# Performance work log

Measured on AMD Instinct MI355X. Metric: run time of the kernel, lower is better.

## Reference

```python
import jax, jax.numpy as jnp
import numpy as np

B, S, D, N, H = 4, 1024, 768, 12, 64
IGNORE = -100000.0


def setup_inputs() -> dict:
    key = jax.random.key(0)
    ks = jax.random.split(key, 9)
    std = 0.02
    return {
        "normalized_resid_pre": jax.random.normal(ks[0], (B, S, D), dtype=jnp.float32),
        "W_Q": jax.random.normal(ks[1], (N, D, H), dtype=jnp.float32) * std,
        "W_K": jax.random.normal(ks[2], (N, D, H), dtype=jnp.float32) * std,
        "W_V": jax.random.normal(ks[3], (N, D, H), dtype=jnp.float32) * std,
        "W_O": jax.random.normal(ks[4], (N, H, D), dtype=jnp.float32) * std,
        "b_Q": jnp.zeros((N, H), dtype=jnp.float32),
        "b_K": jnp.zeros((N, H), dtype=jnp.float32),
        "b_V": jnp.zeros((N, H), dtype=jnp.float32),
        "b_O": jnp.zeros((D,), dtype=jnp.float32),
    }


def reference(normalized_resid_pre, W_Q, W_K, W_V, W_O, b_Q, b_K, b_V, b_O):
    x = normalized_resid_pre  # [b, s, d]
    d_head = W_Q.shape[-1]
    # per-head projections: [b, n, s, h]
    Q = jnp.einsum("bsd,ndh->bnsh", x, W_Q) + b_Q[None, :, None, :]
    K = jnp.einsum("bsd,ndh->bnsh", x, W_K) + b_K[None, :, None, :]
    V = jnp.einsum("bsd,ndh->bnsh", x, W_V) + b_V[None, :, None, :]
    # scores [b, n, s_q, s_k]
    scores = jnp.einsum("bnqh,bnkh->bnqk", Q, K) / jnp.sqrt(jnp.float32(d_head))
    s = scores.shape[-1]
    # original: tril(scores) + triu(IGNORE, k=1) == where(causal, scores, IGNORE)
    causal = jnp.tril(jnp.ones((s, s), dtype=bool))
    masked = jnp.where(causal[None, None], scores, jnp.float32(IGNORE))
    probs = jax.nn.softmax(masked, axis=-1)
    # z [b, s_q, n, h]
    z = jnp.einsum("bnqk,bnkh->bqnh", probs, V)
    out = jnp.einsum("bqnh,nhd->bqd", z, W_O) + b_O
    return out
```

## Files before the change

kernel.cpp:

```cpp
#include <hip/hip_runtime.h>

typedef __bf16 bf16x8 __attribute__((ext_vector_type(8)));
typedef __bf16 bf16x4 __attribute__((ext_vector_type(4)));
typedef float  f32x4  __attribute__((ext_vector_type(4)));

constexpr int B_ = 4, S_ = 1024, D_ = 768, N_ = 12, H_ = 64;
constexpr int BNSH = B_ * N_ * S_ * H_;
constexpr float SCALE2 = 0.18033688011f;

__device__ __forceinline__ f32x4 mfma16(bf16x8 a, bf16x8 b, f32x4 c) {
    return __builtin_amdgcn_mfma_f32_16x16x32_bf16(a, b, c, 0, 0, 0);
}

__device__ __forceinline__ void gload16(const __bf16* g, __bf16* l) {
    __builtin_amdgcn_global_load_lds(
        (const __attribute__((address_space(1))) unsigned int*)g,
        (__attribute__((address_space(3))) unsigned int*)l, 16, 0, 0);
}

__device__ __forceinline__ void stage128x64(const __bf16* g, int ld, __bf16* lds,
                                            int wid, int lane) {
    #pragma unroll
    for (int i = 0; i < 4; ++i) {
        int cb = (wid * 4 + i) * 64;
        int chunk = cb + lane;
        int r = chunk >> 3, p = chunk & 7;
        int q = p ^ (r & 7);
        gload16(g + (size_t)r * ld + q * 8, lds + cb * 8);
    }
}
__device__ __forceinline__ void stage64x64(const __bf16* g, int ld, __bf16* lds,
                                           int wid, int lane) {
    #pragma unroll
    for (int i = 0; i < 2; ++i) {
        int cb = (wid * 2 + i) * 64;
        int chunk = cb + lane;
        int r = chunk >> 3, p = chunk & 7;
        int q = p ^ (r & 7);
        gload16(g + (size_t)r * ld + q * 8, lds + cb * 8);
    }
}

__global__ __launch_bounds__(256) void prep_kernel(
    const float* __restrict__ x,
    const float* __restrict__ wq, const float* __restrict__ wk,
    const float* __restrict__ wv, const float* __restrict__ wo,
    __bf16* __restrict__ xb, __bf16* __restrict__ wt, __bf16* __restrict__ wot) {
    __shared__ __bf16 T[64][65];
    const int blk = blockIdx.x;
    const int tid = threadIdx.x;
    if (blk < 768) {
        int base = blk * 1024 + tid;
        #pragma unroll
        for (int i = 0; i < 4; ++i) {
            int idx = base + i * 256;
            float4 v = ((const float4*)x)[idx];
            bf16x4 o;
            o[0] = (__bf16)v.x; o[1] = (__bf16)v.y;
            o[2] = (__bf16)v.z; o[3] = (__bf16)v.w;
            ((bf16x4*)xb)[idx] = o;
        }
        return;
    }
    int rr = tid >> 4, c4 = (tid & 15) * 4;
    if (blk < 1200) {
        int t = blk - 768;
        int dt = t % 12, mh = t / 12;
        int mat = mh / 12, n = mh % 12;
        const float* in = (mat == 0 ? wq : mat == 1 ? wk : wv) + (size_t)n * 768 * 64;
        __bf16* outp = wt + (size_t)(mat * 768 + n * 64) * 768;
        int d0 = dt * 64;
        #pragma unroll
        for (int i = 0; i < 4; ++i) {
            int row = rr + 16 * i;
            float4 v = *(const float4*)&in[(size_t)(d0 + row) * 64 + c4];
            T[c4 + 0][row] = (__bf16)v.x;
            T[c4 + 1][row] = (__bf16)v.y;
            T[c4 + 2][row] = (__bf16)v.z;
            T[c4 + 3][row] = (__bf16)v.w;
        }
        __syncthreads();
        #pragma unroll
        for (int i = 0; i < 4; ++i) {
            int hrow = rr + 16 * i;
            bf16x4 o;
            o[0] = T[hrow][c4 + 0]; o[1] = T[hrow][c4 + 1];
            o[2] = T[hrow][c4 + 2]; o[3] = T[hrow][c4 + 3];
            *(bf16x4*)&outp[(size_t)hrow * 768 + d0 + c4] = o;
        }
    } else {
        int t = blk - 1200;
        int r0 = (t % 12) * 64, c0 = (t / 12) * 64;
        #pragma unroll
        for (int i = 0; i < 4; ++i) {
            int row = rr + 16 * i;
            float4 v = *(const float4*)&wo[(size_t)(r0 + row) * 768 + c0 + c4];
            T[c4 + 0][row] = (__bf16)v.x;
            T[c4 + 1][row] = (__bf16)v.y;
            T[c4 + 2][row] = (__bf16)v.z;
            T[c4 + 3][row] = (__bf16)v.w;
        }
        __syncthreads();
        #pragma unroll
        for (int i = 0; i < 4; ++i) {
            int crow = rr + 16 * i;
            bf16x4 o;
            o[0] = T[crow][c4 + 0]; o[1] = T[crow][c4 + 1];
            o[2] = T[crow][c4 + 2]; o[3] = T[crow][c4 + 3];
            *(bf16x4*)&wot[(size_t)(c0 + crow) * 768 + r0 + c4] = o;
        }
    }
}

__global__ __launch_bounds__(256) void qkv_gemm(
    const __bf16* __restrict__ xb, const __bf16* __restrict__ wtg,
    const float* __restrict__ bq, const float* __restrict__ bk,
    const float* __restrict__ bv,
    __bf16* __restrict__ Qb, __bf16* __restrict__ Kb, __bf16* __restrict__ Vtb) {
    __shared__ __bf16 As[2][128 * 64];
    __shared__ __bf16 Bs[2][64 * 64];
    const int m0 = blockIdx.x * 128;
    const int j0 = blockIdx.y * 64;
    const int tid = threadIdx.x, wid = tid >> 6, lane = tid & 63;
    const int quad = lane >> 4, lrow = lane & 15;
    const int l3 = lrow & 7;
    int koff[2];
    #pragma unroll
    for (int ks = 0; ks < 2; ++ks)
        koff[ks] = lrow * 64 + ((ks * 4 + quad) ^ l3) * 8;

    f32x4 zf = {0.f, 0.f, 0.f, 0.f};
    f32x4 acc[2][4];
    #pragma unroll
    for (int i = 0; i < 2; ++i)
        #pragma unroll
        for (int j = 0; j < 4; ++j) acc[i][j] = zf;

    stage128x64(xb + (size_t)m0 * 768, 768, As[0], wid, lane);
    stage64x64(wtg + (size_t)j0 * 768, 768, Bs[0], wid, lane);

    for (int kt = 0; kt < 12; ++kt) {
        const int buf = kt & 1;
        __syncthreads();
        if (kt < 11) {
            stage128x64(xb + (size_t)m0 * 768 + (kt + 1) * 64, 768, As[buf ^ 1], wid, lane);
            stage64x64(wtg + (size_t)j0 * 768 + (kt + 1) * 64, 768, Bs[buf ^ 1], wid, lane);
        }
        #pragma unroll
        for (int ks = 0; ks < 2; ++ks) {
            bf16x8 af[2], bfr[4];
            #pragma unroll
            for (int mi = 0; mi < 2; ++mi)
                af[mi] = *(const bf16x8*)(As[buf] + (wid * 32 + mi * 16) * 64 + koff[ks]);
            #pragma unroll
            for (int ni = 0; ni < 4; ++ni)
                bfr[ni] = *(const bf16x8*)(Bs[buf] + ni * 1024 + koff[ks]);
            #pragma unroll
            for (int mi = 0; mi < 2; ++mi)
                #pragma unroll
                for (int ni = 0; ni < 4; ++ni)
                    acc[mi][ni] = mfma16(af[mi], bfr[ni], acc[mi][ni]);
        }
    }

    const int mat = j0 / 768;
    const int n = (j0 % 768) >> 6;
    const int b = m0 >> 10;
    const int s_base = (m0 & 1023) + wid * 32;
    const float* bias = (mat == 0 ? bq : mat == 1 ? bk : bv) + n * 64;
    const float osc = (mat == 0) ? SCALE2 : 1.0f;
    float bias_v[4];
    #pragma unroll
    for (int ni = 0; ni < 4; ++ni) bias_v[ni] = bias[ni * 16 + lrow];

    if (mat == 2) {
        __bf16* vout = Vtb + (size_t)(b * N_ + n) * 64 * 1024;
        #pragma unroll
        for (int mi = 0; mi < 2; ++mi)
            #pragma unroll
            for (int ni = 0; ni < 4; ++ni) {
                int h = ni * 16 + lrow;
                int s0 = s_base + mi * 16 + quad * 4;
                bf16x4 pv;
                #pragma unroll
                for (int r = 0; r < 4; ++r)
                    pv[r] = (__bf16)(acc[mi][ni][r] + bias_v[ni]);
                *(bf16x4*)(vout + (size_t)h * 1024 + s0) = pv;
            }
    } else {
        __bf16* qk = (mat == 0 ? Qb : Kb) + (size_t)(b * N_ + n) * 1024 * 64;
        #pragma unroll
        for (int mi = 0; mi < 2; ++mi)
            #pragma unroll
            for (int r = 0; r < 4; ++r) {
                int s = s_base + mi * 16 + quad * 4 + r;
                #pragma unroll
                for (int ni = 0; ni < 4; ++ni)
                    qk[(size_t)s * 64 + ni * 16 + lrow] =
                        (__bf16)((acc[mi][ni][r] + bias_v[ni]) * osc);
            }
    }
}

__global__ __launch_bounds__(256) void attn_mfma(
    const __bf16* __restrict__ Qb, const __bf16* __restrict__ Kb,
    const __bf16* __restrict__ Vtb, __bf16* __restrict__ zb) {
    __shared__ __bf16 Ks[2][64 * 64], Vs[2][64 * 64];
    __shared__ __bf16 Pt[4][16 * 64];
    const int bid = blockIdx.x;
    const int qt = 15 - bid / 48;
    const int bn = bid % 48;
    const int b = bn / N_, n = bn % N_;
    const int tid = threadIdx.x, wid = tid >> 6, lane = tid & 63;
    const int quad = lane >> 4, lrow = lane & 15;
    const int l3 = lrow & 7;
    const __bf16* Qg = Qb + (size_t)(b * N_ + n) * S_ * H_;
    const __bf16* Kg = Kb + (size_t)(b * N_ + n) * S_ * H_;
    const __bf16* Vg = Vtb + (size_t)(b * N_ + n) * H_ * S_;
    const int q0 = qt * 64;

    int koff[2];
    #pragma unroll
    for (int ks = 0; ks < 2; ++ks)
        koff[ks] = lrow * 64 + ((ks * 4 + quad) ^ l3) * 8;
    int ptw[4], ptr_[2];
    #pragma unroll
    for (int nt = 0; nt < 4; ++nt) {
        int c16 = nt * 2 + (quad >> 1);
        ptw[nt] = lrow * 64 + (c16 ^ l3) * 8 + (quad & 1) * 4;
    }
    #pragma unroll
    for (int ks = 0; ks < 2; ++ks)
        ptr_[ks] = lrow * 64 + ((ks * 4 + quad) ^ l3) * 8;

    bf16x8 qf[2];
    #pragma unroll
    for (int ks = 0; ks < 2; ++ks)
        qf[ks] = *(const bf16x8*)&Qg[(size_t)(q0 + wid * 16 + lrow) * 64
                                     + ks * 32 + quad * 8];

    stage64x64(Kg, 64, Ks[0], wid, lane);
    stage64x64(Vg, 1024, Vs[0], wid, lane);

    f32x4 zf = {0.f, 0.f, 0.f, 0.f};
    f32x4 o[4];
    #pragma unroll
    for (int i = 0; i < 4; ++i) o[i] = zf;
    float m_r = -1e30f, l_r = 0.f;
    __bf16* Pw = Pt[wid];
    const int myq = wid * 16 + lrow;

    auto do_tile = [&](int buf, bool diag) {
        f32x4 sc[4];
        #pragma unroll
        for (int nt = 0; nt < 4; ++nt) sc[nt] = zf;
        #pragma unroll
        for (int ks = 0; ks < 2; ++ks) {
            #pragma unroll
            for (int nt = 0; nt < 4; ++nt) {
                bf16x8 kfr = *(const bf16x8*)(Ks[buf] + nt * 1024 + koff[ks]);
                sc[nt] = mfma16(kfr, qf[ks], sc[nt]);
            }
        }
        if (diag) {
            #pragma unroll
            for (int nt = 0; nt < 4; ++nt)
                #pragma unroll
                for (int r = 0; r < 4; ++r)
                    if ((nt * 16 + quad * 4 + r) > myq) sc[nt][r] = -1e30f;
        }
        float mt = -1e30f;
        #pragma unroll
        for (int nt = 0; nt < 4; ++nt)
            #pragma unroll
            for (int r = 0; r < 4; ++r) mt = fmaxf(mt, sc[nt][r]);
        mt = fmaxf(mt, __shfl_xor(mt, 16));
        mt = fmaxf(mt, __shfl_xor(mt, 32));
        float mn = fmaxf(m_r, mt);
        float alpha = __builtin_amdgcn_exp2f(m_r - mn);
        m_r = mn;
        float rs = 0.f;
        #pragma unroll
        for (int nt = 0; nt < 4; ++nt)
            #pragma unroll
            for (int r = 0; r < 4; ++r) {
                float p = __builtin_amdgcn_exp2f(sc[nt][r] - mn);
                sc[nt][r] = p;
                rs += p;
            }
        rs += __shfl_xor(rs, 16);
        rs += __shfl_xor(rs, 32);
        l_r = l_r * alpha + rs;
        #pragma unroll
        for (int ht = 0; ht < 4; ++ht)
            #pragma unroll
            for (int r = 0; r < 4; ++r) o[ht][r] *= alpha;
        #pragma unroll
        for (int nt = 0; nt < 4; ++nt) {
            bf16x4 pk;
            #pragma unroll
            for (int r = 0; r < 4; ++r) pk[r] = (__bf16)sc[nt][r];
            *(bf16x4*)(Pw + ptw[nt]) = pk;
        }
        #pragma unroll
        for (int ks = 0; ks < 2; ++ks) {
            bf16x8 pf = *(const bf16x8*)(Pw + ptr_[ks]);
            #pragma unroll
            for (int ht = 0; ht < 4; ++ht) {
                bf16x8 vfr = *(const bf16x8*)(Vs[buf] + ht * 1024 + koff[ks]);
                o[ht] = mfma16(vfr, pf, o[ht]);
            }
        }
    };

    for (int kt = 0; kt < qt; ++kt) {
        __syncthreads();
        stage64x64(Kg + (size_t)(kt + 1) * 64 * 64, 64, Ks[(kt + 1) & 1], wid, lane);
        stage64x64(Vg + (kt + 1) * 64, 1024, Vs[(kt + 1) & 1], wid, lane);
        do_tile(kt & 1, false);
    }
    __syncthreads();
    do_tile(qt & 1, true);

    const float linv = 1.0f / l_r;
    __bf16* zout = zb + (size_t)b * S_ * 768 + (size_t)(q0 + myq) * 768 + n * 64;
    #pragma unroll
    for (int ht = 0; ht < 4; ++ht) {
        bf16x4 zo;
        #pragma unroll
        for (int r = 0; r < 4; ++r) zo[r] = (__bf16)(o[ht][r] * linv);
        *(bf16x4*)&zout[ht * 16 + quad * 4] = zo;
    }
}

__global__ __launch_bounds__(256) void out_gemm(
    const __bf16* __restrict__ zb, const __bf16* __restrict__ wot,
    const float* __restrict__ bo, float* __restrict__ out) {
    __shared__ __bf16 As[2][128 * 64];
    __shared__ __bf16 Bs[2][64 * 64];
    const int m0 = blockIdx.x * 128;
    const int j0 = blockIdx.y * 64;
    const int tid = threadIdx.x, wid = tid >> 6, lane = tid & 63;
    const int quad = lane >> 4, lrow = lane & 15;
    const int l3 = lrow & 7;
    int koff[2];
    #pragma unroll
    for (int ks = 0; ks < 2; ++ks)
        koff[ks] = lrow * 64 + ((ks * 4 + quad) ^ l3) * 8;

    f32x4 zf = {0.f, 0.f, 0.f, 0.f};
    f32x4 acc[2][4];
    #pragma unroll
    for (int i = 0; i < 2; ++i)
        #pragma unroll
        for (int j = 0; j < 4; ++j) acc[i][j] = zf;

    stage128x64(zb + (size_t)m0 * 768, 768, As[0], wid, lane);
    stage64x64(wot + (size_t)j0 * 768, 768, Bs[0], wid, lane);

    for (int kt = 0; kt < 12; ++kt) {
        const int buf = kt & 1;
        __syncthreads();
        if (kt < 11) {
            stage128x64(zb + (size_t)m0 * 768 + (kt + 1) * 64, 768, As[buf ^ 1], wid, lane);
            stage64x64(wot + (size_t)j0 * 768 + (kt + 1) * 64, 768, Bs[buf ^ 1], wid, lane);
        }
        #pragma unroll
        for (int ks = 0; ks < 2; ++ks) {
            bf16x8 af[2], bfr[4];
            #pragma unroll
            for (int mi = 0; mi < 2; ++mi)
                af[mi] = *(const bf16x8*)(As[buf] + (wid * 32 + mi * 16) * 64 + koff[ks]);
            #pragma unroll
            for (int ni = 0; ni < 4; ++ni)
                bfr[ni] = *(const bf16x8*)(Bs[buf] + ni * 1024 + koff[ks]);
            #pragma unroll
            for (int mi = 0; mi < 2; ++mi)
                #pragma unroll
                for (int ni = 0; ni < 4; ++ni)
                    acc[mi][ni] = mfma16(af[mi], bfr[ni], acc[mi][ni]);
        }
    }

    float bias_v[4];
    #pragma unroll
    for (int ni = 0; ni < 4; ++ni) bias_v[ni] = bo[j0 + ni * 16 + lrow];
    #pragma unroll
    for (int mi = 0; mi < 2; ++mi)
        #pragma unroll
        for (int r = 0; r < 4; ++r) {
            int m = m0 + wid * 32 + mi * 16 + quad * 4 + r;
            #pragma unroll
            for (int ni = 0; ni < 4; ++ni)
                out[(size_t)m * 768 + j0 + ni * 16 + lrow] =
                    acc[mi][ni][r] + bias_v[ni];
        }
}

extern "C" void kernel_launch(void* const* d_in, const int* in_sizes, int n_in,
                              void* d_out, int out_size, void* d_ws, size_t ws_size,
                              hipStream_t stream) {
    const float* x  = (const float*)d_in[0];
    const float* wq = (const float*)d_in[1];
    const float* wk = (const float*)d_in[2];
    const float* wv = (const float*)d_in[3];
    const float* wo = (const float*)d_in[4];
    const float* bq = (const float*)d_in[5];
    const float* bk = (const float*)d_in[6];
    const float* bv = (const float*)d_in[7];
    const float* bo = (const float*)d_in[8];
    float* out = (float*)d_out;

    __bf16* p   = (__bf16*)d_ws;
    __bf16* xb  = p;  p += (size_t)4096 * 768;
    __bf16* wt  = p;  p += (size_t)2304 * 768;
    __bf16* wot = p;  p += (size_t)768 * 768;
    __bf16* Qb  = p;  p += (size_t)BNSH;
    __bf16* Kb  = p;  p += (size_t)BNSH;
    __bf16* Vtb = p;  p += (size_t)BNSH;
    __bf16* zb  = p;  p += (size_t)4096 * 768;

    prep_kernel<<<1344, 256, 0, stream>>>(x, wq, wk, wv, wo, xb, wt, wot);
    qkv_gemm<<<dim3(32, 36), 256, 0, stream>>>(xb, wt, bq, bk, bv, Qb, Kb, Vtb);
    attn_mfma<<<768, 256, 0, stream>>>(Qb, Kb, Vtb, zb);
    out_gemm<<<dim3(32, 12), 256, 0, stream>>>(zb, wot, bo, out);
}
```

Measured before the change: 143.3 us.

## Load K and V fragments directly from global into registers in attention

The attention kernel no longer stages K and V tiles into shared memory through double-buffered LDS loads with block barriers. Each wave now reads its K and V MFMA fragments straight from global memory into registers, prefetching the next K tile in a register ping-pong. This removes the __syncthreads and LDS traffic, but all four waves now fetch the same K/V data separately from cache. It also raises register pressure and exposes global load latency for V, which is loaded at the start of each tile.

```diff
diff --git a/kernel.cpp b/kernel.cpp
--- a/kernel.cpp
+++ b/kernel.cpp
@@ -205,7 +205,6 @@
 __global__ __launch_bounds__(256) void attn_mfma(
     const __bf16* __restrict__ Qb, const __bf16* __restrict__ Kb,
     const __bf16* __restrict__ Vtb, __bf16* __restrict__ zb) {
-    __shared__ __bf16 Ks[2][64 * 64], Vs[2][64 * 64];
     __shared__ __bf16 Pt[4][16 * 64];
     const int bid = blockIdx.x;
     const int qt = 15 - bid / 48;
@@ -219,10 +218,6 @@
     const __bf16* Vg = Vtb + (size_t)(b * N_ + n) * H_ * S_;
     const int q0 = qt * 64;
 
-    int koff[2];
-    #pragma unroll
-    for (int ks = 0; ks < 2; ++ks)
-        koff[ks] = lrow * 64 + ((ks * 4 + quad) ^ l3) * 8;
     int ptw[4], ptr_[2];
     #pragma unroll
     for (int nt = 0; nt < 4; ++nt) {
@@ -238,9 +233,6 @@
     for (int ks = 0; ks < 2; ++ks)
         qf[ks] = *(const bf16x8*)&Qg[(size_t)(q0 + wid * 16 + lrow) * 64
                                      + ks * 32 + quad * 8];
-
-    stage64x64(Kg, 64, Ks[0], wid, lane);
-    stage64x64(Vg, 1024, Vs[0], wid, lane);
 
     f32x4 zf = {0.f, 0.f, 0.f, 0.f};
     f32x4 o[4];
@@ -250,19 +242,33 @@
     __bf16* Pw = Pt[wid];
     const int myq = wid * 16 + lrow;
 
-    auto do_tile = [&](int buf, bool diag) {
+    auto load_kf = [&](int kt, bf16x8* dst) {
+        #pragma unroll
+        for (int ks = 0; ks < 2; ++ks)
+            #pragma unroll
+            for (int nt = 0; nt < 4; ++nt)
+                dst[ks * 4 + nt] = *(const bf16x8*)&Kg[
+                    (size_t)(kt * 64 + nt * 16 + lrow) * 64 + ks * 32 + quad * 8];
+    };
+
+    auto tile = [&](int kt, bf16x8* kc, bf16x8* kn) {
+        bf16x8 vf[8];
+        #pragma unroll
+        for (int ks = 0; ks < 2; ++ks)
+            #pragma unroll
+            for (int ht = 0; ht < 4; ++ht)
+                vf[ks * 4 + ht] = *(const bf16x8*)&Vg[
+                    (size_t)(ht * 16 + lrow) * 1024 + kt * 64 + ks * 32 + quad * 8];
         f32x4 sc[4];
         #pragma unroll
         for (int nt = 0; nt < 4; ++nt) sc[nt] = zf;
         #pragma unroll
-        for (int ks = 0; ks < 2; ++ks) {
-            #pragma unroll
-            for (int nt = 0; nt < 4; ++nt) {
-                bf16x8 kfr = *(const bf16x8*)(Ks[buf] + nt * 1024 + koff[ks]);
-                sc[nt] = mfma16(kfr, qf[ks], sc[nt]);
-            }
-        }
-        if (diag) {
+        for (int ks = 0; ks < 2; ++ks)
+            #pragma unroll
+            for (int nt = 0; nt < 4; ++nt)
+                sc[nt] = mfma16(kc[ks * 4 + nt], qf[ks], sc[nt]);
+        if (kt + 1 <= qt) load_kf(kt + 1, kn);
+        if (kt == qt) {
             #pragma unroll
             for (int nt = 0; nt < 4; ++nt)
                 #pragma unroll
@@ -306,21 +312,17 @@
         for (int ks = 0; ks < 2; ++ks) {
             bf16x8 pf = *(const bf16x8*)(Pw + ptr_[ks]);
             #pragma unroll
-            for (int ht = 0; ht < 4; ++ht) {
-                bf16x8 vfr = *(const bf16x8*)(Vs[buf] + ht * 1024 + koff[ks]);
-                o[ht] = mfma16(vfr, pf, o[ht]);
-            }
+            for (int ht = 0; ht < 4; ++ht)
+                o[ht] = mfma16(vf[ks * 4 + ht], pf, o[ht]);
         }
     };
 
-    for (int kt = 0; kt < qt; ++kt) {
-        __syncthreads();
-        stage64x64(Kg + (size_t)(kt + 1) * 64 * 64, 64, Ks[(kt + 1) & 1], wid, lane);
-        stage64x64(Vg + (kt + 1) * 64, 1024, Vs[(kt + 1) & 1], wid, lane);
-        do_tile(kt & 1, false);
-    }
-    __syncthreads();
-    do_tile(qt & 1, true);
+    bf16x8 kf[8], kf2[8];
+    load_kf(0, kf);
+    for (int kt = 0; kt <= qt; kt += 2) {
+        tile(kt, kf, kf2);
+        if (kt + 1 <= qt) tile(kt + 1, kf2, kf);
+    }
 
     const float linv = 1.0f / l_r;
     __bf16* zout = zb + (size_t)b * S_ * 768 + (size_t)(q0 + myq) * 768 + n * 64;
```

Result: slower. 175.5 us (+22.4%).
